# Optimization experiments

Measured on AMD Instinct MI355X. Metric: run time of the kernel, lower is better.

Reference implementation:

```python
import jax, jax.numpy as jnp
import numpy as np

B, N, D = 8, 256, 128   # batch, nodes, feature width
MID, OUT = 128, 128
FEAT = 2 * D            # concat(n_features, hidden)


def _glorot(key, fan_in, fan_out):
    s = (2.0 / (fan_in + fan_out)) ** 0.5
    return jax.random.normal(key, (fan_in, fan_out), dtype=jnp.float32) * s


def setup_inputs() -> dict:
    key = jax.random.key(0)
    ks = jax.random.split(key, 12)
    inp = {
        "hidden": jax.random.normal(ks[0], (B, N, D), dtype=jnp.float32),
        "n_features": jax.random.normal(ks[1], (B, N, D), dtype=jnp.float32),
        "e_features": jax.random.normal(ks[2], (B, N, N, D), dtype=jnp.float32),
        "g_features": jax.random.normal(ks[3], (B, D), dtype=jnp.float32),
        "adj": jax.random.bernoulli(ks[4], 0.5, (B, N, N)).astype(jnp.float32),
        # Linear params (haiku Linear: y = x @ w + b)
        "W1": _glorot(ks[5], FEAT, MID), "b1": jnp.zeros((MID,), jnp.float32),
        "W2": _glorot(ks[6], FEAT, MID), "b2": jnp.zeros((MID,), jnp.float32),
        "We": _glorot(ks[7], D, MID),    "be": jnp.zeros((MID,), jnp.float32),
        "Wg": _glorot(ks[8], D, MID),    "bg": jnp.zeros((MID,), jnp.float32),
        "Wo1": _glorot(ks[9], FEAT, OUT), "bo1": jnp.zeros((OUT,), jnp.float32),
        "Wo2": _glorot(ks[10], MID, OUT), "bo2": jnp.zeros((OUT,), jnp.float32),
    }
    return inp


def reference(hidden, n_features, e_features, g_features, adj,
              W1, b1, W2, b2, We, be, Wg, bg, Wo1, bo1, Wo2, bo2):
    # features: (B, N, 2D)
    features = jnp.concatenate([n_features, hidden], axis=-1)
    msg_1 = features @ W1 + b1              # (B, N, MID)
    msg_2 = features @ W2 + b2              # (B, N, MID)
    msg_e = e_features @ We + be            # (B, N, N, MID)
    msg_g = g_features @ Wg + bg            # (B, MID)
    # broadcast-add: msgs[b, i, j] = msg_1[b, j] + msg_2[b, i] + msg_e[b, i, j] + msg_g[b]
    msgs = (msg_1[:, None, :, :] + msg_2[:, :, None, :]
            + msg_e + msg_g[:, None, None, :])  # (B, N, N, MID)
    # masked max reduction over axis=1 (default reduction=jnp.max branch)
    msgs = jnp.max(msgs * adj[..., None], axis=1)  # (B, N, MID)
    ret = (features @ Wo1 + bo1) + (msgs @ Wo2 + bo2)  # (B, N, OUT)
    return ret
```

## Files before the change

kernel.cpp:

```cpp
#include <hip/hip_runtime.h>
#include <stdint.h>

#define B_   8
#define N_   256
#define D_   128
#define MID_ 128
#define FEAT_ 256

typedef __attribute__((ext_vector_type(4))) float  floatx4;
typedef __attribute__((ext_vector_type(4))) int    intx4;
typedef __attribute__((ext_vector_type(8))) __bf16 bf16x8;

__device__ __forceinline__ floatx4 mfma16(bf16x8 a, bf16x8 b, floatx4 c) {
    return __builtin_amdgcn_mfma_f32_16x16x32_bf16(a, b, c, 0, 0, 0);
}

__device__ __forceinline__ bf16x8 cvt8(floatx4 a, floatx4 b) {
    bf16x8 r;
    r[0] = (__bf16)a[0]; r[1] = (__bf16)a[1]; r[2] = (__bf16)a[2]; r[3] = (__bf16)a[3];
    r[4] = (__bf16)b[0]; r[5] = (__bf16)b[1]; r[6] = (__bf16)b[2]; r[7] = (__bf16)b[3];
    return r;
}

__global__ void __launch_bounds__(256)
kW(const float* __restrict__ W1, const float* __restrict__ W2,
   const float* __restrict__ Wo1, const float* __restrict__ We,
   __bf16* __restrict__ dst) {
    int t = threadIdx.x;
    int g = blockIdx.x * 2 + (t >> 7);
    int m = t & 127;
    const float* src; int kg; int off;
    if (g < 32)      { src = W1;  kg = g;      off = 0; }
    else if (g < 64) { src = W2;  kg = g - 32; off = 32768; }
    else if (g < 96) { src = Wo1; kg = g - 64; off = 65536; }
    else             { src = We;  kg = g - 96; off = 98304; }
    bf16x8 r;
#pragma unroll
    for (int jv = 0; jv < 8; ++jv) r[jv] = (__bf16)src[(kg * 8 + jv) * MID_ + m];
    int base = (((kg >> 2) * 8 + (m >> 4)) * 64 + (kg & 3) * 16 + (m & 15)) * 8;
    *(bf16x8*)&dst[off + base] = r;
}

__global__ void __launch_bounds__(256)
kA(const float* __restrict__ nfeat, const float* __restrict__ hidden,
   const __bf16* __restrict__ Wpre,
   const float* __restrict__ g, const float* __restrict__ Wg,
   const float* __restrict__ bg, const float* __restrict__ b1,
   const float* __restrict__ be, const float* __restrict__ b2,
   const float* __restrict__ bo1, const float* __restrict__ bo2,
   float* __restrict__ C, float* __restrict__ msg2, float* __restrict__ retA) {
    __shared__ __bf16 Wb[8 * 8 * 64 * 8];
    __shared__ float gp_part[2][MID_];
    __shared__ float gp_sh[MID_];
    int t = threadIdx.x;
    int wid = blockIdx.y;
    {
        const intx4* srcW = (const intx4*)(Wpre + (size_t)wid * 32768);
        intx4* dstW = (intx4*)Wb;
#pragma unroll
        for (int it = 0; it < 16; ++it) dstW[t + it * 256] = srcW[t + it * 256];
    }
    int bblk = blockIdx.x >> 2;
    if (wid == 0) {
        int m = t & 127, h = t >> 7;
        const float* gr = g + bblk * D_;
        float a = 0.f;
        for (int k = h * 64; k < h * 64 + 64; ++k)
            a += gr[k] * Wg[k * MID_ + m];
        gp_part[h][m] = a;
    }
    __syncthreads();
    if (wid == 0 && t < 128)
        gp_sh[t] = gp_part[0][t] + gp_part[1][t] + bg[t] + b1[t] + be[t];
    __syncthreads();

    int lane = t & 63, w = t >> 6;
    int n16 = lane & 15, quad = lane >> 4;
    int R = blockIdx.x * 64 + w * 16 + n16;
    const float* frow0 = nfeat  + (size_t)R * D_ + quad * 8;
    const float* frow1 = hidden + (size_t)R * D_ + quad * 8;

    bf16x8 bfrag[8];
#pragma unroll
    for (int ks = 0; ks < 8; ++ks) {
        const float* p = (ks < 4) ? (frow0 + ks * 32) : (frow1 + (ks - 4) * 32);
        floatx4 v0 = *(const floatx4*)p;
        floatx4 v1 = *(const floatx4*)(p + 4);
        bfrag[ks] = cvt8(v0, v1);
    }

    float* outp = (wid == 0) ? C : ((wid == 1) ? msg2 : retA);
#pragma unroll 2
    for (int mt = 0; mt < 8; ++mt) {
        floatx4 acc = (floatx4)0.f;
#pragma unroll
        for (int ks = 0; ks < 8; ++ks) {
            bf16x8 a = *(const bf16x8*)&Wb[((ks * 8 + mt) * 64 + lane) * 8];
            acc = mfma16(a, bfrag[ks], acc);
        }
        int m0 = mt * 16 + quad * 4;
        floatx4 add;
        if (wid == 0)      add = *(const floatx4*)&gp_sh[m0];
        else if (wid == 1) add = *(const floatx4*)&b2[m0];
        else {
            floatx4 x = *(const floatx4*)&bo1[m0];
            floatx4 y = *(const floatx4*)&bo2[m0];
            add = x + y;
        }
        *(floatx4*)&outp[(size_t)R * MID_ + m0] = acc + add;
    }
}

__global__ void __launch_bounds__(256, 4)
kB(const float* __restrict__ e, const __bf16* __restrict__ Wes,
   const float* __restrict__ adj, const float* __restrict__ C,
   const float* __restrict__ msg2, const float* __restrict__ retA,
   const float* __restrict__ Wo2, float* __restrict__ out) {
    __shared__ __bf16 Wb[4 * 8 * 64 * 8];
    __shared__ float C_sh[MID_];
    __shared__ float wmax[4][MID_];
    __shared__ float msgs_sh[MID_];
    __shared__ float part[2][MID_];
    __shared__ unsigned short list_sh[N_];
    __shared__ float aval_sh[N_];
    __shared__ int wcnt[4];

    int t = threadIdx.x;
    int b = blockIdx.x >> 7, j0 = (blockIdx.x & 127) << 1;
    int lane = t & 63, w = t >> 6;
    int n16 = lane & 15, quad = lane >> 4;

    {
        const intx4* srcW = (const intx4*)Wes;
        intx4* dstW = (intx4*)Wb;
#pragma unroll
        for (int it = 0; it < 8; ++it) dstW[t + it * 256] = srcW[t + it * 256];
    }
    float2 av2 = *(const float2*)&adj[(size_t)b * N_ * N_ + (size_t)t * N_ + j0];

    const size_t erow = (size_t)N_ * D_;
    const float* m2b = msg2 + (size_t)b * N_ * MID_;

    for (int jj = 0; jj < 2; ++jj) {
        int j = j0 + jj;
        float av = jj ? av2.y : av2.x;
        bool act = (av != 0.f);
        unsigned long long mk = __ballot(act);
        if (lane == 0) wcnt[w] = __popcll(mk);
        if (t < 128) C_sh[t] = C[((size_t)b * N_ + j) * MID_ + t];
        __syncthreads();
        int nact = wcnt[0] + wcnt[1] + wcnt[2] + wcnt[3];
        int base = 0;
        if (w > 0) base += wcnt[0];
        if (w > 1) base += wcnt[1];
        if (w > 2) base += wcnt[2];
        int pos = base + __popcll(mk & ((1ull << lane) - 1ull));
        if (act) { list_sh[pos] = (unsigned short)t; aval_sh[pos] = av; }
        __syncthreads();

        const float* ebase = e + (size_t)b * N_ * N_ * D_ + (size_t)j * D_ + quad * 8;

        floatx4 rm[8];
#pragma unroll
        for (int mt = 0; mt < 8; ++mt) rm[mt] = (floatx4)(-INFINITY);

        int nch = (nact + 15) >> 4;
        for (int c = w; c < nch; c += 8) {
            int s0 = c * 16 + n16;
            int s1 = (c + 4) * 16 + n16;
            int i0 = 0, i1 = 0; float aw0 = 0.f, aw1 = 0.f;
            if (s0 < nact) { i0 = list_sh[s0]; aw0 = aval_sh[s0]; }
            if (s1 < nact) { i1 = list_sh[s1]; aw1 = aval_sh[s1]; }
            const float* r0 = ebase + (size_t)i0 * erow;
            const float* r1 = ebase + (size_t)i1 * erow;
            bf16x8 ef0[4], ef1[4];
#pragma unroll
            for (int q = 0; q < 4; ++q) {
                floatx4 a0 = *(const floatx4*)(r0 + q * 32);
                floatx4 b0 = *(const floatx4*)(r0 + q * 32 + 4);
                floatx4 a1 = *(const floatx4*)(r1 + q * 32);
                floatx4 b1 = *(const floatx4*)(r1 + q * 32 + 4);
                ef0[q] = cvt8(a0, b0);
                ef1[q] = cvt8(a1, b1);
            }
            const float* m2r0 = m2b + (size_t)i0 * MID_;
            const float* m2r1 = m2b + (size_t)i1 * MID_;
#pragma unroll 2
            for (int mt = 0; mt < 8; ++mt) {
                int m0 = mt * 16 + quad * 4;
                floatx4 c4 = *(const floatx4*)&C_sh[m0];
                floatx4 acc0 = c4, acc1 = c4;
#pragma unroll
                for (int ks = 0; ks < 4; ++ks) {
                    bf16x8 aW = *(const bf16x8*)&Wb[((ks * 8 + mt) * 64 + lane) * 8];
                    acc0 = mfma16(aW, ef0[ks], acc0);
                    acc1 = mfma16(aW, ef1[ks], acc1);
                }
                floatx4 m20 = *(const floatx4*)&m2r0[m0];
                floatx4 m21 = *(const floatx4*)&m2r1[m0];
#pragma unroll
                for (int r = 0; r < 4; ++r) {
                    float v0 = (acc0[r] + m20[r]) * aw0;
                    float v1 = (acc1[r] + m21[r]) * aw1;
                    rm[mt][r] = fmaxf(rm[mt][r], fmaxf(v0, v1));
                }
            }
        }

#pragma unroll
        for (int mt = 0; mt < 8; ++mt) {
#pragma unroll
            for (int r = 0; r < 4; ++r) {
                float v = rm[mt][r];
                v = fmaxf(v, __shfl_xor(v, 1, 64));
                v = fmaxf(v, __shfl_xor(v, 2, 64));
                v = fmaxf(v, __shfl_xor(v, 4, 64));
                v = fmaxf(v, __shfl_xor(v, 8, 64));
                rm[mt][r] = v;
            }
        }
        if (n16 == 0) {
#pragma unroll
            for (int mt = 0; mt < 8; ++mt)
                *(floatx4*)&wmax[w][mt * 16 + quad * 4] = rm[mt];
        }
        __syncthreads();

        int m = t & 127, h = t >> 7;
        if (t < 128) {
            float mx = fmaxf(fmaxf(wmax[0][m], wmax[1][m]), fmaxf(wmax[2][m], wmax[3][m]));
            if (nact < 256) mx = fmaxf(mx, 0.f);
            msgs_sh[m] = mx;
        }
        __syncthreads();

        float a2 = 0.f;
        for (int k = h * 64; k < h * 64 + 64; ++k)
            a2 += msgs_sh[k] * Wo2[k * MID_ + m];
        part[h][m] = a2;
        __syncthreads();
        if (t < 128) {
            int R = b * N_ + j;
            out[(size_t)R * MID_ + m] = retA[R * MID_ + m] + part[0][m] + part[1][m];
        }
        __syncthreads();
    }
}

extern "C" void kernel_launch(void* const* d_in, const int* in_sizes, int n_in,
                              void* d_out, int out_size, void* d_ws, size_t ws_size,
                              hipStream_t stream) {
    (void)in_sizes; (void)n_in; (void)out_size; (void)ws_size;
    const float* hidden = (const float*)d_in[0];
    const float* nfeat  = (const float*)d_in[1];
    const float* e      = (const float*)d_in[2];
    const float* g      = (const float*)d_in[3];
    const float* adj    = (const float*)d_in[4];
    const float* W1  = (const float*)d_in[5];
    const float* b1  = (const float*)d_in[6];
    const float* W2  = (const float*)d_in[7];
    const float* b2  = (const float*)d_in[8];
    const float* We  = (const float*)d_in[9];
    const float* be  = (const float*)d_in[10];
    const float* Wg  = (const float*)d_in[11];
    const float* bg  = (const float*)d_in[12];
    const float* Wo1 = (const float*)d_in[13];
    const float* bo1 = (const float*)d_in[14];
    const float* Wo2 = (const float*)d_in[15];
    const float* bo2 = (const float*)d_in[16];
    float* outp = (float*)d_out;

    float* ws = (float*)d_ws;
    __bf16* Wpre = (__bf16*)ws;
    float* C    = ws + 57344;
    float* msg2 = C + 262144;
    float* retA = msg2 + 262144;

    kW<<<56, 256, 0, stream>>>(W1, W2, Wo1, We, Wpre);
    kA<<<dim3(32, 3), 256, 0, stream>>>(nfeat, hidden, Wpre,
                                        g, Wg, bg, b1, be, b2, bo1, bo2,
                                        C, msg2, retA);
    kB<<<1024, 256, 0, stream>>>(e, Wpre + 98304, adj, C, msg2, retA, Wo2, outp);
}
```

Baseline: 428.2 us.

## Assign one column per block and software-pipeline edge row loads

Each block of kB now handles a single output column j instead of two, and the grid doubles to 2048 blocks. The inner loop processes one 16-row chunk per wave per iteration and prefetches the next chunk's e_features rows into registers while the current chunk's MFMAs run. This is meant to hide global load latency on the dominant e_features stream and give more blocks for parallelism. In exchange the Wb shared-memory copy of the weights is reloaded twice as often, and less independent MFMA work is in flight per iteration.

```diff
diff --git a/kernel.cpp b/kernel.cpp
--- a/kernel.cpp
+++ b/kernel.cpp
@@ -126,7 +126,7 @@
     __shared__ int wcnt[4];
 
     int t = threadIdx.x;
-    int b = blockIdx.x >> 7, j0 = (blockIdx.x & 127) << 1;
+    int b = blockIdx.x >> 8, j = blockIdx.x & 255;
     int lane = t & 63, w = t >> 6;
     int n16 = lane & 15, quad = lane >> 4;
 
@@ -136,114 +136,119 @@
 #pragma unroll
         for (int it = 0; it < 8; ++it) dstW[t + it * 256] = srcW[t + it * 256];
     }
-    float2 av2 = *(const float2*)&adj[(size_t)b * N_ * N_ + (size_t)t * N_ + j0];
+    float av = adj[(size_t)b * N_ * N_ + (size_t)t * N_ + j];
+    bool act = (av != 0.f);
+    unsigned long long mk = __ballot(act);
+    if (lane == 0) wcnt[w] = __popcll(mk);
+    if (t < 128) C_sh[t] = C[((size_t)b * N_ + j) * MID_ + t];
+    __syncthreads();
+    int nact = wcnt[0] + wcnt[1] + wcnt[2] + wcnt[3];
+    int base = 0;
+    if (w > 0) base += wcnt[0];
+    if (w > 1) base += wcnt[1];
+    if (w > 2) base += wcnt[2];
+    int pos = base + __popcll(mk & ((1ull << lane) - 1ull));
+    if (act) { list_sh[pos] = (unsigned short)t; aval_sh[pos] = av; }
+    __syncthreads();
 
     const size_t erow = (size_t)N_ * D_;
-    const float* m2b = msg2 + (size_t)b * N_ * MID_;
-
-    for (int jj = 0; jj < 2; ++jj) {
-        int j = j0 + jj;
-        float av = jj ? av2.y : av2.x;
-        bool act = (av != 0.f);
-        unsigned long long mk = __ballot(act);
-        if (lane == 0) wcnt[w] = __popcll(mk);
-        if (t < 128) C_sh[t] = C[((size_t)b * N_ + j) * MID_ + t];
-        __syncthreads();
-        int nact = wcnt[0] + wcnt[1] + wcnt[2] + wcnt[3];
-        int base = 0;
-        if (w > 0) base += wcnt[0];
-        if (w > 1) base += wcnt[1];
-        if (w > 2) base += wcnt[2];
-        int pos = base + __popcll(mk & ((1ull << lane) - 1ull));
-        if (act) { list_sh[pos] = (unsigned short)t; aval_sh[pos] = av; }
-        __syncthreads();
-
-        const float* ebase = e + (size_t)b * N_ * N_ * D_ + (size_t)j * D_ + quad * 8;
-
-        floatx4 rm[8];
-#pragma unroll
-        for (int mt = 0; mt < 8; ++mt) rm[mt] = (floatx4)(-INFINITY);
-
-        int nch = (nact + 15) >> 4;
-        for (int c = w; c < nch; c += 8) {
-            int s0 = c * 16 + n16;
-            int s1 = (c + 4) * 16 + n16;
-            int i0 = 0, i1 = 0; float aw0 = 0.f, aw1 = 0.f;
-            if (s0 < nact) { i0 = list_sh[s0]; aw0 = aval_sh[s0]; }
-            if (s1 < nact) { i1 = list_sh[s1]; aw1 = aval_sh[s1]; }
-            const float* r0 = ebase + (size_t)i0 * erow;
-            const float* r1 = ebase + (size_t)i1 * erow;
-            bf16x8 ef0[4], ef1[4];
+    const float* ebase = e + (size_t)b * N_ * N_ * D_ + (size_t)j * D_ + quad * 8;
+    const float* m2b   = msg2 + (size_t)b * N_ * MID_;
+
+    floatx4 rm[8];
+#pragma unroll
+    for (int mt = 0; mt < 8; ++mt) rm[mt] = (floatx4)(-INFINITY);
+
+    int nch = (nact + 15) >> 4;
+
+    int idxn = 0; float awn = 0.f;
+    {
+        int slot = w * 16 + n16;
+        if (w < nch && slot < nact) { idxn = list_sh[slot]; awn = aval_sh[slot]; }
+    }
+    floatx4 v[8];
+    {
+        const float* rowp = ebase + (size_t)idxn * erow;
+#pragma unroll
+        for (int q = 0; q < 4; ++q) {
+            v[2 * q]     = *(const floatx4*)(rowp + q * 32);
+            v[2 * q + 1] = *(const floatx4*)(rowp + q * 32 + 4);
+        }
+    }
+
+    for (int c = w; c < nch; c += 4) {
+        bf16x8 ef[4];
+#pragma unroll
+        for (int q = 0; q < 4; ++q) ef[q] = cvt8(v[2 * q], v[2 * q + 1]);
+        float aw = awn;
+        const float* m2r = m2b + (size_t)idxn * MID_;
+
+        int cn = c + 4;
+        idxn = 0; awn = 0.f;
+        {
+            int slot = cn * 16 + n16;
+            if (cn < nch && slot < nact) { idxn = list_sh[slot]; awn = aval_sh[slot]; }
+        }
+        {
+            const float* rowp = ebase + (size_t)idxn * erow;
 #pragma unroll
             for (int q = 0; q < 4; ++q) {
-                floatx4 a0 = *(const floatx4*)(r0 + q * 32);
-                floatx4 b0 = *(const floatx4*)(r0 + q * 32 + 4);
-                floatx4 a1 = *(const floatx4*)(r1 + q * 32);
-                floatx4 b1 = *(const floatx4*)(r1 + q * 32 + 4);
-                ef0[q] = cvt8(a0, b0);
-                ef1[q] = cvt8(a1, b1);
+                v[2 * q]     = *(const floatx4*)(rowp + q * 32);
+                v[2 * q + 1] = *(const floatx4*)(rowp + q * 32 + 4);
             }
-            const float* m2r0 = m2b + (size_t)i0 * MID_;
-            const float* m2r1 = m2b + (size_t)i1 * MID_;
+        }
+
 #pragma unroll 2
-            for (int mt = 0; mt < 8; ++mt) {
-                int m0 = mt * 16 + quad * 4;
-                floatx4 c4 = *(const floatx4*)&C_sh[m0];
-                floatx4 acc0 = c4, acc1 = c4;
-#pragma unroll
-                for (int ks = 0; ks < 4; ++ks) {
-                    bf16x8 aW = *(const bf16x8*)&Wb[((ks * 8 + mt) * 64 + lane) * 8];
-                    acc0 = mfma16(aW, ef0[ks], acc0);
-                    acc1 = mfma16(aW, ef1[ks], acc1);
-                }
-                floatx4 m20 = *(const floatx4*)&m2r0[m0];
-                floatx4 m21 = *(const floatx4*)&m2r1[m0];
-#pragma unroll
-                for (int r = 0; r < 4; ++r) {
-                    float v0 = (acc0[r] + m20[r]) * aw0;
-                    float v1 = (acc1[r] + m21[r]) * aw1;
-                    rm[mt][r] = fmaxf(rm[mt][r], fmaxf(v0, v1));
-                }
+        for (int mt = 0; mt < 8; ++mt) {
+            int m0 = mt * 16 + quad * 4;
+            floatx4 m2v = *(const floatx4*)&m2r[m0];
+            floatx4 acc = *(const floatx4*)&C_sh[m0];
+#pragma unroll
+            for (int ks = 0; ks < 4; ++ks) {
+                bf16x8 aW = *(const bf16x8*)&Wb[((ks * 8 + mt) * 64 + lane) * 8];
+                acc = mfma16(aW, ef[ks], acc);
             }
-        }
-
-#pragma unroll
-        for (int mt = 0; mt < 8; ++mt) {
-#pragma unroll
-            for (int r = 0; r < 4; ++r) {
-                float v = rm[mt][r];
-                v = fmaxf(v, __shfl_xor(v, 1, 64));
-                v = fmaxf(v, __shfl_xor(v, 2, 64));
-                v = fmaxf(v, __shfl_xor(v, 4, 64));
-                v = fmaxf(v, __shfl_xor(v, 8, 64));
-                rm[mt][r] = v;
-            }
-        }
-        if (n16 == 0) {
-#pragma unroll
-            for (int mt = 0; mt < 8; ++mt)
-                *(floatx4*)&wmax[w][mt * 16 + quad * 4] = rm[mt];
-        }
-        __syncthreads();
-
-        int m = t & 127, h = t >> 7;
-        if (t < 128) {
-            float mx = fmaxf(fmaxf(wmax[0][m], wmax[1][m]), fmaxf(wmax[2][m], wmax[3][m]));
-            if (nact < 256) mx = fmaxf(mx, 0.f);
-            msgs_sh[m] = mx;
-        }
-        __syncthreads();
-
-        float a2 = 0.f;
-        for (int k = h * 64; k < h * 64 + 64; ++k)
-            a2 += msgs_sh[k] * Wo2[k * MID_ + m];
-        part[h][m] = a2;
-        __syncthreads();
-        if (t < 128) {
-            int R = b * N_ + j;
-            out[(size_t)R * MID_ + m] = retA[R * MID_ + m] + part[0][m] + part[1][m];
-        }
-        __syncthreads();
+#pragma unroll
+            for (int r = 0; r < 4; ++r)
+                rm[mt][r] = fmaxf(rm[mt][r], (acc[r] + m2v[r]) * aw);
+        }
+    }
+
+#pragma unroll
+    for (int mt = 0; mt < 8; ++mt) {
+#pragma unroll
+        for (int r = 0; r < 4; ++r) {
+            float vv = rm[mt][r];
+            vv = fmaxf(vv, __shfl_xor(vv, 1, 64));
+            vv = fmaxf(vv, __shfl_xor(vv, 2, 64));
+            vv = fmaxf(vv, __shfl_xor(vv, 4, 64));
+            vv = fmaxf(vv, __shfl_xor(vv, 8, 64));
+            rm[mt][r] = vv;
+        }
+    }
+    if (n16 == 0) {
+#pragma unroll
+        for (int mt = 0; mt < 8; ++mt)
+            *(floatx4*)&wmax[w][mt * 16 + quad * 4] = rm[mt];
+    }
+    __syncthreads();
+
+    int m = t & 127, h = t >> 7;
+    if (t < 128) {
+        float mx = fmaxf(fmaxf(wmax[0][m], wmax[1][m]), fmaxf(wmax[2][m], wmax[3][m]));
+        if (nact < 256) mx = fmaxf(mx, 0.f);
+        msgs_sh[m] = mx;
+    }
+    __syncthreads();
+
+    float a2 = 0.f;
+    for (int k = h * 64; k < h * 64 + 64; ++k)
+        a2 += msgs_sh[k] * Wo2[k * MID_ + m];
+    part[h][m] = a2;
+    __syncthreads();
+    if (t < 128) {
+        int R = b * N_ + j;
+        out[(size_t)R * MID_ + m] = retA[R * MID_ + m] + part[0][m] + part[1][m];
     }
 }
 
@@ -280,5 +285,5 @@
     kA<<<dim3(32, 3), 256, 0, stream>>>(nfeat, hidden, Wpre,
                                         g, Wg, bg, b1, be, b2, bo1, bo2,
                                         C, msg2, retA);
-    kB<<<1024, 256, 0, stream>>>(e, Wpre + 98304, adj, C, msg2, retA, Wo2, outp);
-}
+    kB<<<2048, 256, 0, stream>>>(e, Wpre + 98304, adj, C, msg2, retA, Wo2, outp);
+}
```

After: 399.9 us. 1.07x faster.
